# Kernel optimization log

Measured on AMD Instinct MI355X. Metric: run time of the kernel, lower is better.

## Reference

```python
import jax, jax.numpy as jnp
import numpy as np


def bilinear_sampler(img, flow):
    """Warp img (B,H,W,C) by per-pixel flow (B,H,W,2): sample at (x+u, y+v).
    Border handling: indices clipped to the image (edge padding)."""
    B, H, W, C = img.shape
    gy, gx = jnp.meshgrid(jnp.arange(H, dtype=img.dtype),
                          jnp.arange(W, dtype=img.dtype), indexing='ij')
    x = gx[None] + flow[..., 0]  # (B,H,W)
    y = gy[None] + flow[..., 1]
    x0f = jnp.floor(x)
    y0f = jnp.floor(y)
    wx = x - x0f  # fractional parts, differentiable w.r.t. flow
    wy = y - y0f
    x0 = jnp.clip(x0f.astype(jnp.int32), 0, W - 1)
    x1 = jnp.clip(x0f.astype(jnp.int32) + 1, 0, W - 1)
    y0 = jnp.clip(y0f.astype(jnp.int32), 0, H - 1)
    y1 = jnp.clip(y0f.astype(jnp.int32) + 1, 0, H - 1)
    b = jnp.arange(B)[:, None, None]
    Ia = img[b, y0, x0]  # (B,H,W,C)
    Ib = img[b, y1, x0]
    Ic = img[b, y0, x1]
    Id = img[b, y1, x1]
    wx = wx[..., None]
    wy = wy[..., None]
    return (Ia * (1 - wx) * (1 - wy) + Ib * (1 - wx) * wy
            + Ic * wx * (1 - wy) + Id * wx * wy)


def setup_inputs() -> dict:
    key = jax.random.key(0)
    k1, k2, k3, k4, k5, k6 = jax.random.split(key, 6)
    B, H, W = 8, 512, 512
    return {
        't': jax.random.uniform(k1, (B, 1, 1, 1), dtype=jnp.float32),
        'I0': jax.random.uniform(k2, (B, H, W, 3), dtype=jnp.float32),
        'I1': jax.random.uniform(k3, (B, H, W, 3), dtype=jnp.float32),
        'interp': jax.random.normal(k4, (B, H, W, 5), dtype=jnp.float32),
        'Fhat_t0': jax.random.normal(k5, (B, H, W, 2), dtype=jnp.float32),
        'Fhat_t1': jax.random.normal(k6, (B, H, W, 2), dtype=jnp.float32),
    }


def reference(t, I0, I1, interp, Fhat_t0, Fhat_t1):
    Ft0 = interp[..., 0:2] + Fhat_t0
    Ft1 = interp[..., 2:4] + Fhat_t1
    Vt0 = jax.nn.sigmoid(interp[..., 4:5])  # (B,H,W,1) -> broadcasts over RGB
    Vt1 = 1.0 - Vt0
    g0 = bilinear_sampler(I0, Ft0)
    g1 = bilinear_sampler(I1, Ft1)
    eps = 1e-12
    w0 = (1.0 - t) * Vt0
    w1 = t * Vt1
    It = (w0 * g0 + w1 * g1) / (w0 + w1 + eps)
    return It
```

## Files before the change

kernel.cpp:

```cpp
#include <hip/hip_runtime.h>

constexpr int B_ = 8;
constexpr int H_ = 512;
constexpr int W_ = 512;
constexpr int HW_ = H_ * W_;

constexpr int TS = 32;
constexpr int R_ = 4;
constexpr int RS = 40;
constexpr int ROWB = RS * 12;
constexpr int PAIRB = 2 * ROWB;


template <int IMG>
__device__ __forceinline__ void sampleT(const char* __restrict__ lds,
                                        const float* __restrict__ img,
                                        int gx0, int gy0,
                                        float sx, float sy, float g[3]) {
    float xf = floorf(sx), yf = floorf(sy);
    float wx = sx - xf, wy = sy - yf;
    int ix = (int)xf, iy = (int)yf;
    int x0 = min(max(ix, 0), W_ - 1);
    int x1 = min(max(ix + 1, 0), W_ - 1);
    int y0 = min(max(iy, 0), H_ - 1);
    int y1 = min(max(iy + 1, 0), H_ - 1);

    float w00 = (1.0f - wx) * (1.0f - wy);
    float w01 = wx * (1.0f - wy);
    float w10 = (1.0f - wx) * wy;
    float w11 = wx * wy;

    int lx0 = x0 - gx0, lx1 = x1 - gx0;
    int ly0 = y0 - gy0, ly1 = y1 - gy0;
    bool inT = ((unsigned)lx0 < (unsigned)RS) & ((unsigned)lx1 < (unsigned)RS) &
               ((unsigned)ly0 < (unsigned)RS) & ((unsigned)ly1 < (unsigned)RS);

    if (inT) {
        const float* t00 = (const float*)(lds + ly0 * PAIRB + IMG * ROWB + lx0 * 12);
        const float* t01 = (const float*)(lds + ly0 * PAIRB + IMG * ROWB + lx1 * 12);
        const float* t10 = (const float*)(lds + ly1 * PAIRB + IMG * ROWB + lx0 * 12);
        const float* t11 = (const float*)(lds + ly1 * PAIRB + IMG * ROWB + lx1 * 12);
        #pragma unroll
        for (int ch = 0; ch < 3; ++ch)
            g[ch] = t00[ch] * w00 + t01[ch] * w01 +
                    t10[ch] * w10 + t11[ch] * w11;
    } else {
        const float* pa = img + ((size_t)y0 * W_ + x0) * 3;
        const float* pb = img + ((size_t)y0 * W_ + x1) * 3;
        const float* pc = img + ((size_t)y1 * W_ + x0) * 3;
        const float* pd = img + ((size_t)y1 * W_ + x1) * 3;
        #pragma unroll
        for (int ch = 0; ch < 3; ++ch)
            g[ch] = pa[ch] * w00 + pb[ch] * w01 +
                    pc[ch] * w10 + pd[ch] * w11;
    }
}

__global__ __launch_bounds__(256, 4) void frame_interp_dma(
    const float* __restrict__ t,
    const float* __restrict__ I0,
    const float* __restrict__ I1,
    const float* __restrict__ interp,
    const float* __restrict__ F0,
    const float* __restrict__ F1,
    float* __restrict__ out)
{
    __shared__ __align__(16) char lds_raw[RS * PAIRB];

    int tid  = threadIdx.x;
    int lane = tid & 63;
    int wave = tid >> 6;
    int bid  = blockIdx.x;
    int b    = bid & 7;
    int tile = bid >> 3;
    int ty   = tile >> 4;
    int tx   = tile & 15;
    int gx0 = min(max(tx * TS - R_, 0), W_ - RS);
    int gy0 = min(max(ty * TS - R_, 0), H_ - RS);

    const float* img0 = I0 + (size_t)b * HW_ * 3;
    const float* img1 = I1 + (size_t)b * HW_ * 3;

    float tb = t[b];

    #pragma unroll
    for (int j = 0; j < 10; ++j) {
        int r  = wave * 10 + j;
        int gy = gy0 + r;
        char* ldsbase = lds_raw + r * PAIRB;
        const char* g0row = (const char*)(img0 + ((size_t)gy * W_ + gx0) * 3);
        const char* g1row = (const char*)(img1 + ((size_t)gy * W_ + gx0) * 3);
        if (lane < 60) {
            const char* src = (lane < 30) ? g0row + lane * 16
                                          : g1row + (lane - 30) * 16;
            __builtin_amdgcn_global_load_lds(
                (const __attribute__((address_space(1))) void*)src,
                (__attribute__((address_space(3))) void*)ldsbase,
                16, 0, 0);
        }
    }

    int row  = tid >> 3;
    int colb = (tid & 7) * 4;
    int gy_o = ty * TS + row;
    int gx_o = tx * TS + colb;
    size_t idx0 = (size_t)b * HW_ + (size_t)gy_o * W_ + gx_o;

    float ii[20], f0v[8], f1v[8];
    __builtin_memcpy(ii, interp + idx0 * 5, 80);
    __builtin_memcpy(f0v, F0 + idx0 * 2, 32);
    __builtin_memcpy(f1v, F1 + idx0 * 2, 32);

    asm volatile("s_waitcnt vmcnt(0)" ::: "memory");
    __syncthreads();

    float o[12];
    #pragma unroll
    for (int k = 0; k < 4; ++k) {
        float fx = (float)(gx_o + k);
        float fy = (float)gy_o;
        float sx0 = fx + ii[k * 5 + 0] + f0v[k * 2 + 0];
        float sy0 = fy + ii[k * 5 + 1] + f0v[k * 2 + 1];
        float sx1 = fx + ii[k * 5 + 2] + f1v[k * 2 + 0];
        float sy1 = fy + ii[k * 5 + 3] + f1v[k * 2 + 1];
        float vt0 = 1.0f / (1.0f + __expf(-ii[k * 5 + 4]));

        float g0[3], g1[3];
        sampleT<0>(lds_raw, img0, gx0, gy0, sx0, sy0, g0);
        sampleT<1>(lds_raw, img1, gx0, gy0, sx1, sy1, g1);

        float w0 = (1.0f - tb) * vt0;
        float w1 = tb * (1.0f - vt0);
        float inv = 1.0f / (w0 + w1 + 1e-12f);
        o[k * 3 + 0] = (w0 * g0[0] + w1 * g1[0]) * inv;
        o[k * 3 + 1] = (w0 * g0[1] + w1 * g1[1]) * inv;
        o[k * 3 + 2] = (w0 * g0[2] + w1 * g1[2]) * inv;
    }
    __builtin_memcpy(out + idx0 * 3, o, 48);
}

extern "C" void kernel_launch(void* const* d_in, const int* in_sizes, int n_in,
                              void* d_out, int out_size, void* d_ws, size_t ws_size,
                              hipStream_t stream) {
    const float* t      = (const float*)d_in[0];
    const float* I0     = (const float*)d_in[1];
    const float* I1     = (const float*)d_in[2];
    const float* interp = (const float*)d_in[3];
    const float* F0     = (const float*)d_in[4];
    const float* F1     = (const float*)d_in[5];
    float* out = (float*)d_out;

    int blocks = B_ * (H_ / TS) * (W_ / TS);
    frame_interp_dma<<<blocks, 256, 0, stream>>>(t, I0, I1, interp, F0, F1, out);
}
```

Measured before the change: 166.4 us.

## Process two tiles per block with double-buffered LDS staging overlap

Each block now handles two horizontally adjacent 32x32 tiles. It issues async global-to-LDS loads for both tiles into two LDS buffers, then computes the first tile after a partial vmcnt wait while the second tile is still loading. The sampler is split into an unconditional, clamped LDS read plus a conditional global fallback, which is meant to cut divergence inside the hot loop. The costs are half as many blocks, launch bounds lowered to 2 blocks per SM, double the LDS per block, and reliance on exact vmcnt accounting for correctness.

```diff
diff --git a/kernel.cpp b/kernel.cpp
--- a/kernel.cpp
+++ b/kernel.cpp
@@ -10,12 +10,10 @@
 constexpr int RS = 40;
 constexpr int ROWB = RS * 12;
 constexpr int PAIRB = 2 * ROWB;
-
-
-template <int IMG>
-__device__ __forceinline__ void sampleT(const char* __restrict__ lds,
-                                        const float* __restrict__ img,
-                                        int gx0, int gy0,
+constexpr int TILEB = RS * PAIRB;
+
+
+__device__ __forceinline__ void sampleG(const float* __restrict__ img,
                                         float sx, float sy, float g[3]) {
     float xf = floorf(sx), yf = floorf(sy);
     float wx = sx - xf, wy = sy - yf;
@@ -24,70 +22,94 @@
     int x1 = min(max(ix + 1, 0), W_ - 1);
     int y0 = min(max(iy, 0), H_ - 1);
     int y1 = min(max(iy + 1, 0), H_ - 1);
-
     float w00 = (1.0f - wx) * (1.0f - wy);
     float w01 = wx * (1.0f - wy);
     float w10 = (1.0f - wx) * wy;
     float w11 = wx * wy;
+    float a[3], bv[3], c[3], d[3];
+    __builtin_memcpy(a,  img + ((size_t)y0 * W_ + x0) * 3, 12);
+    __builtin_memcpy(bv, img + ((size_t)y0 * W_ + x1) * 3, 12);
+    __builtin_memcpy(c,  img + ((size_t)y1 * W_ + x0) * 3, 12);
+    __builtin_memcpy(d,  img + ((size_t)y1 * W_ + x1) * 3, 12);
+    #pragma unroll
+    for (int ch = 0; ch < 3; ++ch)
+        g[ch] = a[ch] * w00 + bv[ch] * w01 + c[ch] * w10 + d[ch] * w11;
+}
+
+template <int IMG>
+__device__ __forceinline__ bool sampleL(const char* lds, int gx0, int gy0,
+                                        float sx, float sy, float g[3]) {
+    float xf = floorf(sx), yf = floorf(sy);
+    float wx = sx - xf, wy = sy - yf;
+    int ix = (int)xf, iy = (int)yf;
+    int x0 = min(max(ix, 0), W_ - 1);
+    int x1 = min(max(ix + 1, 0), W_ - 1);
+    int y0 = min(max(iy, 0), H_ - 1);
+    int y1 = min(max(iy + 1, 0), H_ - 1);
+    float w00 = (1.0f - wx) * (1.0f - wy);
+    float w01 = wx * (1.0f - wy);
+    float w10 = (1.0f - wx) * wy;
+    float w11 = wx * wy;
 
     int lx0 = x0 - gx0, lx1 = x1 - gx0;
     int ly0 = y0 - gy0, ly1 = y1 - gy0;
-    bool inT = ((unsigned)lx0 < (unsigned)RS) & ((unsigned)lx1 < (unsigned)RS) &
-               ((unsigned)ly0 < (unsigned)RS) & ((unsigned)ly1 < (unsigned)RS);
-
-    if (inT) {
-        const float* t00 = (const float*)(lds + ly0 * PAIRB + IMG * ROWB + lx0 * 12);
-        const float* t01 = (const float*)(lds + ly0 * PAIRB + IMG * ROWB + lx1 * 12);
-        const float* t10 = (const float*)(lds + ly1 * PAIRB + IMG * ROWB + lx0 * 12);
-        const float* t11 = (const float*)(lds + ly1 * PAIRB + IMG * ROWB + lx1 * 12);
-        #pragma unroll
-        for (int ch = 0; ch < 3; ++ch)
-            g[ch] = t00[ch] * w00 + t01[ch] * w01 +
-                    t10[ch] * w10 + t11[ch] * w11;
-    } else {
-        const float* pa = img + ((size_t)y0 * W_ + x0) * 3;
-        const float* pb = img + ((size_t)y0 * W_ + x1) * 3;
-        const float* pc = img + ((size_t)y1 * W_ + x0) * 3;
-        const float* pd = img + ((size_t)y1 * W_ + x1) * 3;
-        #pragma unroll
-        for (int ch = 0; ch < 3; ++ch)
-            g[ch] = pa[ch] * w00 + pb[ch] * w01 +
-                    pc[ch] * w10 + pd[ch] * w11;
+    bool ok = ((unsigned)lx0 < (unsigned)RS) & ((unsigned)lx1 < (unsigned)RS) &
+              ((unsigned)ly0 < (unsigned)RS) & ((unsigned)ly1 < (unsigned)RS);
+    lx0 = min(max(lx0, 0), RS - 1);
+    lx1 = min(max(lx1, 0), RS - 1);
+    ly0 = min(max(ly0, 0), RS - 1);
+    ly1 = min(max(ly1, 0), RS - 1);
+
+    const float* t00 = (const float*)(lds + ly0 * PAIRB + IMG * ROWB + lx0 * 12);
+    const float* t01 = (const float*)(lds + ly0 * PAIRB + IMG * ROWB + lx1 * 12);
+    const float* t10 = (const float*)(lds + ly1 * PAIRB + IMG * ROWB + lx0 * 12);
+    const float* t11 = (const float*)(lds + ly1 * PAIRB + IMG * ROWB + lx1 * 12);
+    #pragma unroll
+    for (int ch = 0; ch < 3; ++ch)
+        g[ch] = t00[ch] * w00 + t01[ch] * w01 + t10[ch] * w10 + t11[ch] * w11;
+    return ok;
+}
+
+__device__ __forceinline__ void computeTile(
+    const char* lds, int gx0, int gy0, int gx_o, int gy_o,
+    const float* __restrict__ img0, const float* __restrict__ img1, float tb,
+    const float ii[20], const float f0v[8], const float f1v[8], float o[12])
+{
+    #pragma unroll
+    for (int k = 0; k < 4; ++k) {
+        float fx = (float)(gx_o + k);
+        float fy = (float)gy_o;
+        float sx0 = fx + ii[k * 5 + 0] + f0v[k * 2 + 0];
+        float sy0 = fy + ii[k * 5 + 1] + f0v[k * 2 + 1];
+        float sx1 = fx + ii[k * 5 + 2] + f1v[k * 2 + 0];
+        float sy1 = fy + ii[k * 5 + 3] + f1v[k * 2 + 1];
+        float vt0 = 1.0f / (1.0f + __expf(-ii[k * 5 + 4]));
+
+        float g0[3], g1[3];
+        bool ok0 = sampleL<0>(lds, gx0, gy0, sx0, sy0, g0);
+        bool ok1 = sampleL<1>(lds, gx0, gy0, sx1, sy1, g1);
+        if (!ok0) sampleG(img0, sx0, sy0, g0);
+        if (!ok1) sampleG(img1, sx1, sy1, g1);
+
+        float w0 = (1.0f - tb) * vt0;
+        float w1 = tb * (1.0f - vt0);
+        float inv = 1.0f / (w0 + w1 + 1e-12f);
+        o[k * 3 + 0] = (w0 * g0[0] + w1 * g1[0]) * inv;
+        o[k * 3 + 1] = (w0 * g0[1] + w1 * g1[1]) * inv;
+        o[k * 3 + 2] = (w0 * g0[2] + w1 * g1[2]) * inv;
     }
 }
 
-__global__ __launch_bounds__(256, 4) void frame_interp_dma(
-    const float* __restrict__ t,
-    const float* __restrict__ I0,
-    const float* __restrict__ I1,
-    const float* __restrict__ interp,
-    const float* __restrict__ F0,
-    const float* __restrict__ F1,
-    float* __restrict__ out)
+__device__ __forceinline__ void stageTile(char* lds,
+                                          const float* __restrict__ img0,
+                                          const float* __restrict__ img1,
+                                          int gx0, int gy0, int wave, int lane)
 {
-    __shared__ __align__(16) char lds_raw[RS * PAIRB];
-
-    int tid  = threadIdx.x;
-    int lane = tid & 63;
-    int wave = tid >> 6;
-    int bid  = blockIdx.x;
-    int b    = bid & 7;
-    int tile = bid >> 3;
-    int ty   = tile >> 4;
-    int tx   = tile & 15;
-    int gx0 = min(max(tx * TS - R_, 0), W_ - RS);
-    int gy0 = min(max(ty * TS - R_, 0), H_ - RS);
-
-    const float* img0 = I0 + (size_t)b * HW_ * 3;
-    const float* img1 = I1 + (size_t)b * HW_ * 3;
-
-    float tb = t[b];
-
     #pragma unroll
     for (int j = 0; j < 10; ++j) {
         int r  = wave * 10 + j;
         int gy = gy0 + r;
-        char* ldsbase = lds_raw + r * PAIRB;
+        char* ldsbase = lds + r * PAIRB;
         const char* g0row = (const char*)(img0 + ((size_t)gy * W_ + gx0) * 3);
         const char* g1row = (const char*)(img1 + ((size_t)gy * W_ + gx0) * 3);
         if (lane < 60) {
@@ -99,44 +121,73 @@
                 16, 0, 0);
         }
     }
+}
+
+__global__ __launch_bounds__(256, 2) void frame_interp_pipe(
+    const float* __restrict__ t,
+    const float* __restrict__ I0,
+    const float* __restrict__ I1,
+    const float* __restrict__ interp,
+    const float* __restrict__ F0,
+    const float* __restrict__ F1,
+    float* __restrict__ out)
+{
+    __shared__ __align__(16) char lds[2][TILEB];
+
+    int tid  = threadIdx.x;
+    int lane = tid & 63;
+    int wave = tid >> 6;
+    int bid  = blockIdx.x;
+    int b   = bid & 7;
+    int sup = bid >> 3;
+    int ty  = sup >> 3;
+    int px  = sup & 7;
+    int txA = px * 2, txB = px * 2 + 1;
+
+    int gy0  = min(max(ty  * TS - R_, 0), H_ - RS);
+    int gx0A = min(max(txA * TS - R_, 0), W_ - RS);
+    int gx0B = min(max(txB * TS - R_, 0), W_ - RS);
+
+    const float* img0 = I0 + (size_t)b * HW_ * 3;
+    const float* img1 = I1 + (size_t)b * HW_ * 3;
+    float tb = t[b];
 
     int row  = tid >> 3;
     int colb = (tid & 7) * 4;
-    int gy_o = ty * TS + row;
-    int gx_o = tx * TS + colb;
-    size_t idx0 = (size_t)b * HW_ + (size_t)gy_o * W_ + gx_o;
-
-    float ii[20], f0v[8], f1v[8];
-    __builtin_memcpy(ii, interp + idx0 * 5, 80);
-    __builtin_memcpy(f0v, F0 + idx0 * 2, 32);
-    __builtin_memcpy(f1v, F1 + idx0 * 2, 32);
+    int gy_o  = ty * TS + row;
+    int gx_oA = txA * TS + colb;
+    size_t idxA = (size_t)b * HW_ + (size_t)gy_o * W_ + gx_oA;
+    size_t idxB = idxA + TS;
+
+    float iiA[20], f0A[8], f1A[8], iiB[20], f0B[8], f1B[8];
+    __builtin_memcpy(iiA, interp + idxA * 5, 80);
+    __builtin_memcpy(f0A, F0 + idxA * 2, 32);
+    __builtin_memcpy(f1A, F1 + idxA * 2, 32);
+    __builtin_memcpy(iiB, interp + idxB * 5, 80);
+    __builtin_memcpy(f0B, F0 + idxB * 2, 32);
+    __builtin_memcpy(f1B, F1 + idxB * 2, 32);
+
+    stageTile(lds[0], img0, img1, gx0A, gy0, wave, lane);
+    stageTile(lds[1], img0, img1, gx0B, gy0, wave, lane);
+
+    asm volatile("s_waitcnt vmcnt(10)" ::: "memory");
+    __builtin_amdgcn_sched_barrier(0);
+    __builtin_amdgcn_s_barrier();
+
+    float oA[12];
+    computeTile(lds[0], gx0A, gy0, gx_oA, gy_o, img0, img1, tb,
+                iiA, f0A, f1A, oA);
 
     asm volatile("s_waitcnt vmcnt(0)" ::: "memory");
-    __syncthreads();
-
-    float o[12];
-    #pragma unroll
-    for (int k = 0; k < 4; ++k) {
-        float fx = (float)(gx_o + k);
-        float fy = (float)gy_o;
-        float sx0 = fx + ii[k * 5 + 0] + f0v[k * 2 + 0];
-        float sy0 = fy + ii[k * 5 + 1] + f0v[k * 2 + 1];
-        float sx1 = fx + ii[k * 5 + 2] + f1v[k * 2 + 0];
-        float sy1 = fy + ii[k * 5 + 3] + f1v[k * 2 + 1];
-        float vt0 = 1.0f / (1.0f + __expf(-ii[k * 5 + 4]));
-
-        float g0[3], g1[3];
-        sampleT<0>(lds_raw, img0, gx0, gy0, sx0, sy0, g0);
-        sampleT<1>(lds_raw, img1, gx0, gy0, sx1, sy1, g1);
-
-        float w0 = (1.0f - tb) * vt0;
-        float w1 = tb * (1.0f - vt0);
-        float inv = 1.0f / (w0 + w1 + 1e-12f);
-        o[k * 3 + 0] = (w0 * g0[0] + w1 * g1[0]) * inv;
-        o[k * 3 + 1] = (w0 * g0[1] + w1 * g1[1]) * inv;
-        o[k * 3 + 2] = (w0 * g0[2] + w1 * g1[2]) * inv;
-    }
-    __builtin_memcpy(out + idx0 * 3, o, 48);
+    __builtin_amdgcn_sched_barrier(0);
+    __builtin_amdgcn_s_barrier();
+
+    float oB[12];
+    computeTile(lds[1], gx0B, gy0, gx_oA + TS, gy_o, img0, img1, tb,
+                iiB, f0B, f1B, oB);
+
+    __builtin_memcpy(out + idxA * 3, oA, 48);
+    __builtin_memcpy(out + idxB * 3, oB, 48);
 }
 
 extern "C" void kernel_launch(void* const* d_in, const int* in_sizes, int n_in,
@@ -150,6 +201,6 @@
     const float* F1     = (const float*)d_in[5];
     float* out = (float*)d_out;
 
-    int blocks = B_ * (H_ / TS) * (W_ / TS);
-    frame_interp_dma<<<blocks, 256, 0, stream>>>(t, I0, I1, interp, F0, F1, out);
-}
+    int blocks = B_ * (H_ / TS) * (W_ / (2 * TS));
+    frame_interp_pipe<<<blocks, 256, 0, stream>>>(t, I0, I1, interp, F0, F1, out);
+}
```

Result: no change. 165.5 us (-0.5%).
